# Optimization experiments

Hardware: AMD Instinct MI355X
Metric: run time of the kernel (lower is better)

The kernel has to match this reference:

```python
import math
import jax, jax.numpy as jnp
import numpy as np

DMODEL = 1024
NUM_HEADS = 16
HEAD_DIM = DMODEL // NUM_HEADS
MAX_LEN = 1024


def setup_inputs() -> dict:
    key = jax.random.key(0)
    ks = jax.random.split(key, 10)
    bs, S = 4, 1024
    s = 0.02
    return {
        "query": jax.random.normal(ks[0], (bs, S, DMODEL), jnp.float32),
        "key": jax.random.normal(ks[1], (bs, S, DMODEL), jnp.float32),
        "value": jax.random.normal(ks[2], (bs, S, DMODEL), jnp.float32),
        "Wq": jax.random.normal(ks[3], (DMODEL, DMODEL), jnp.float32) * s,
        "bq": jnp.zeros((DMODEL,), jnp.float32),
        "Wk": jax.random.normal(ks[4], (DMODEL, DMODEL), jnp.float32) * s,
        "bk": jnp.zeros((DMODEL,), jnp.float32),
        "Wv": jax.random.normal(ks[5], (DMODEL, DMODEL), jnp.float32) * s,
        "bv": jnp.zeros((DMODEL,), jnp.float32),
        # relative embedding table: (H, 2*max_len-1+2, head_dim)
        "Er": jax.random.normal(ks[6], (NUM_HEADS, 2 * MAX_LEN + 1, HEAD_DIM), jnp.float32),
    }


def _skew(QEr):
    # Music-Transformer skew trick. QEr: (bs, H, S, L) with L = 2S-1.
    bs, H, S, L = QEr.shape
    x = jnp.pad(QEr, ((0, 0), (0, 0), (0, 0), (0, 1)))          # (bs,H,S,L+1)
    x = x.reshape(bs, H, S * (L + 1))
    x = jnp.pad(x, ((0, 0), (0, 0), (0, L - S)))
    x = x.reshape(bs, H, S + 1, L)
    return x[:, :, :S, -S:]                                      # (bs,H,S,S)


def reference(query, key, value, Wq, bq, Wk, bk, Wv, bv, Er):
    bs, S, D = query.shape
    H, hd = NUM_HEADS, HEAD_DIM
    # torch nn.Linear: x @ W.T + b
    q = (query @ Wq.T + bq).reshape(bs, S, H, hd).transpose(0, 2, 1, 3)  # (bs,H,S,hd)
    k = (key @ Wk.T + bk).reshape(bs, S, H, hd).transpose(0, 2, 1, 3)    # (bs,H,S,hd)
    v = (value @ Wv.T + bv).reshape(bs, S, H, hd).transpose(0, 2, 1, 3)  # (bs,H,S,hd)
    # slice Er for src_len <= max_len: rows [max_len-S, max_len+S-1) -> (H, 2S-1, hd)
    Er_t = Er[:, max(0, MAX_LEN - S):min(2 * MAX_LEN - 1, MAX_LEN + S - 1), :]
    QEr = jnp.einsum('bhsd,hld->bhsl', q, Er_t)                  # (bs,H,S,2S-1)
    Srel = _skew(QEr)                                            # (bs,H,S,S)
    attn = (jnp.einsum('bhsd,bhtd->bhst', q, k) + Srel) / math.sqrt(hd)
    attn = jax.nn.softmax(attn, axis=-1)
    out = jnp.einsum('bhst,bhtd->bhsd', attn, v)                 # (bs,H,S,hd)
    out = out.transpose(0, 2, 1, 3).reshape(bs, S, D)
    return out, attn
```

## Files before the change

### kernel.cpp

```cpp
#include <hip/hip_runtime.h>
#include <hip/hip_fp16.h>

#define SQ   1024
#define DM   1024
#define NH   16
#define HD   64
#define BSZ  4
#define MROW 4096

typedef _Float16 f16;
typedef f16  f16x8 __attribute__((ext_vector_type(8)));
typedef float f32x4 __attribute__((ext_vector_type(4)));

#define MFMA16(a,b,c) __builtin_amdgcn_mfma_f32_16x16x32_f16(a,b,c,0,0,0)

#define XIN16OFF  0
#define W16OFF    12582912
#define ER16OFF   15728640
#define QKV16OFF  17826816

__global__ __launch_bounds__(256) void cvt_all(
    const float* __restrict__ q, const float* __restrict__ k, const float* __restrict__ v,
    const float* __restrict__ wq, const float* __restrict__ wk, const float* __restrict__ wv,
    const float* __restrict__ er, f16* __restrict__ ws)
{
    int z = blockIdx.z;
    const float* src; f16* dst; int n;
    if (z < 3)      { src = (z==0)?q:((z==1)?k:v);    dst = ws + (size_t)z*4194304;              n = 4194304; }
    else if (z < 6) { src = (z==3)?wq:((z==4)?wk:wv); dst = ws + W16OFF + (size_t)(z-3)*1048576; n = 1048576; }
    else            { src = er;                        dst = ws + ER16OFF;                        n = 2098176; }
    int idx = (blockIdx.x*256 + threadIdx.x) * 8;
    if (idx >= n) return;
    float4 a = *(const float4*)&src[idx];
    float4 b = *(const float4*)&src[idx+4];
    f16x8 o;
    o[0]=(f16)a.x; o[1]=(f16)a.y; o[2]=(f16)a.z; o[3]=(f16)a.w;
    o[4]=(f16)b.x; o[5]=(f16)b.y; o[6]=(f16)b.z; o[7]=(f16)b.w;
    *(f16x8*)&dst[idx] = o;
}

__global__ __launch_bounds__(256) void proj_gemm(
    f16* __restrict__ ws, const float* __restrict__ bq,
    const float* __restrict__ bk, const float* __restrict__ bv)
{
    int z = blockIdx.z;
    const f16* X = ws + XIN16OFF + (size_t)z*4194304;
    const f16* W = ws + W16OFF   + (size_t)z*1048576;
    const float* bias = (z==0)?bq:((z==1)?bk:bv);
    f16* dst = ws + QKV16OFF + (size_t)z*4194304;

    int n0 = blockIdx.x * 64, m0 = blockIdx.y * 64;
    int tid = threadIdx.x, lane = tid & 63, w = tid >> 6;
    int wm = (w >> 1) * 32, wn = (w & 1) * 32;

    __shared__ f16 As[64*40];
    __shared__ f16 Bs[64*40];

    f32x4 acc[2][2];
    #pragma unroll
    for (int a=0;a<2;++a) for (int b=0;b<2;++b) { acc[a][b][0]=0.f;acc[a][b][1]=0.f;acc[a][b][2]=0.f;acc[a][b][3]=0.f; }

    int row = tid >> 2, kc = (tid & 3) * 8;
    int fr = lane & 15, fk = (lane >> 4) << 3;

    for (int k0 = 0; k0 < 1024; k0 += 32) {
        __syncthreads();
        *(f16x8*)&As[row*40 + kc] = *(const f16x8*)&X[(size_t)(m0+row)*1024 + k0 + kc];
        *(f16x8*)&Bs[row*40 + kc] = *(const f16x8*)&W[(size_t)(n0+row)*1024 + k0 + kc];
        __syncthreads();
        f16x8 af[2], bf[2];
        af[0] = *(const f16x8*)&As[(wm +      fr)*40 + fk];
        af[1] = *(const f16x8*)&As[(wm + 16 + fr)*40 + fk];
        bf[0] = *(const f16x8*)&Bs[(wn +      fr)*40 + fk];
        bf[1] = *(const f16x8*)&Bs[(wn + 16 + fr)*40 + fk];
        #pragma unroll
        for (int a=0;a<2;++a)
            #pragma unroll
            for (int b=0;b<2;++b)
                acc[a][b] = MFMA16(af[a], bf[b], acc[a][b]);
    }

    int coln = lane & 15, rq = (lane >> 4) << 2;
    #pragma unroll
    for (int bb = 0; bb < 2; ++bb) {
        int j = n0 + wn + bb*16 + coln;
        int hh = j >> 6, dd = j & 63;
        float bsv = bias[j];
        #pragma unroll
        for (int a = 0; a < 2; ++a) {
            #pragma unroll
            for (int r = 0; r < 4; ++r) {
                int m = m0 + wm + a*16 + rq + r;
                int bidx = m >> 10, s = m & 1023;
                dst[((size_t)(bidx*16 + hh)*1024 + s)*64 + dd] = (f16)(acc[a][bb][r] + bsv);
            }
        }
    }
}

__global__ __launch_bounds__(256) void attn_kernel(
    const f16* __restrict__ ws, float* __restrict__ attn)
{
    const f16* qkv = ws + QKV16OFF;
    const f16* er  = ws + ER16OFF;
    int bh = blockIdx.y;
    int h  = bh & 15;
    int s0 = blockIdx.x << 4;
    int tid = threadIdx.x, lane = tid & 63, w = tid >> 6;

    const f16* qb = qkv + (size_t)bh * 65536;
    const f16* kb = qkv + 4194304 + (size_t)bh * 65536;
    const f16* E  = er + (size_t)h * 2049 * 64;

    int fr = lane & 15, fk = (lane >> 4) << 3;
    f16x8 qf0 = *(const f16x8*)&qb[(s0+fr)*64 + fk];
    f16x8 qf1 = *(const f16x8*)&qb[(s0+fr)*64 + fk + 32];

    int tbase = w << 8;
    f32x4 sc[16];
    int l0 = 1008 + tbase - s0;
    f16x8 e0a = *(const f16x8*)&E[(size_t)(l0+fr)*64 + fk];
    f16x8 e0b = *(const f16x8*)&E[(size_t)(l0+fr)*64 + fk + 32];

    #pragma unroll
    for (int i = 0; i < 16; ++i) {
        int t0 = tbase + (i << 4);
        f16x8 kf0 = *(const f16x8*)&kb[(t0+fr)*64 + fk];
        f16x8 kf1 = *(const f16x8*)&kb[(t0+fr)*64 + fk + 32];
        f32x4 c; c[0]=0.f;c[1]=0.f;c[2]=0.f;c[3]=0.f;
        c = MFMA16(qf0, kf0, c);
        c = MFMA16(qf1, kf1, c);

        int l1 = l0 + 16;
        f16x8 e1a = *(const f16x8*)&E[(size_t)(l1+fr)*64 + fk];
        f16x8 e1b = *(const f16x8*)&E[(size_t)(l1+fr)*64 + fk + 32];
        f32x4 r0; r0[0]=0.f;r0[1]=0.f;r0[2]=0.f;r0[3]=0.f;
        f32x4 r1; r1[0]=0.f;r1[1]=0.f;r1[2]=0.f;r1[3]=0.f;
        r0 = MFMA16(qf0, e0a, r0); r0 = MFMA16(qf1, e0b, r0);
        r1 = MFMA16(qf0, e1a, r1); r1 = MFMA16(qf1, e1b, r1);

        #pragma unroll
        for (int r = 0; r < 4; ++r) {
            int shat = ((lane >> 4) << 2) + r;
            int jj = (lane & 15) - shat + 15;
            int addr = ((lane & 48) | (jj & 15)) << 2;
            float g0 = __int_as_float(__builtin_amdgcn_ds_bpermute(addr, __float_as_int(r0[r])));
            float g1 = __int_as_float(__builtin_amdgcn_ds_bpermute(addr, __float_as_int(r1[r])));
            c[r] = (c[r] + ((jj < 16) ? g0 : g1)) * 0.125f;
        }
        sc[i] = c;
        e0a = e1a; e0b = e1b; l0 = l1;
    }

    __shared__ float red[16][4];
    float mx[4];
    #pragma unroll
    for (int r = 0; r < 4; ++r) {
        float m = sc[0][r];
        #pragma unroll
        for (int i = 1; i < 16; ++i) m = fmaxf(m, sc[i][r]);
        m = fmaxf(m, __shfl_xor(m, 1));
        m = fmaxf(m, __shfl_xor(m, 2));
        m = fmaxf(m, __shfl_xor(m, 4));
        m = fmaxf(m, __shfl_xor(m, 8));
        mx[r] = m;
    }
    if ((lane & 15) == 0) {
        #pragma unroll
        for (int r = 0; r < 4; ++r) red[((lane>>4)<<2)+r][w] = mx[r];
    }
    __syncthreads();
    #pragma unroll
    for (int r = 0; r < 4; ++r) {
        int rw = ((lane>>4)<<2)+r;
        mx[r] = fmaxf(fmaxf(red[rw][0], red[rw][1]), fmaxf(red[rw][2], red[rw][3]));
    }
    __syncthreads();
    float sm[4];
    #pragma unroll
    for (int r = 0; r < 4; ++r) {
        float s = 0.f;
        #pragma unroll
        for (int i = 0; i < 16; ++i) { float e = __expf(sc[i][r] - mx[r]); sc[i][r] = e; s += e; }
        s += __shfl_xor(s, 1); s += __shfl_xor(s, 2);
        s += __shfl_xor(s, 4); s += __shfl_xor(s, 8);
        sm[r] = s;
    }
    if ((lane & 15) == 0) {
        #pragma unroll
        for (int r = 0; r < 4; ++r) red[((lane>>4)<<2)+r][w] = sm[r];
    }
    __syncthreads();
    float inv[4];
    #pragma unroll
    for (int r = 0; r < 4; ++r) {
        int rw = ((lane>>4)<<2)+r;
        inv[r] = 1.f / (red[rw][0] + red[rw][1] + red[rw][2] + red[rw][3]);
    }

    float* outb = attn + ((size_t)bh * 1024 + s0) * 1024;
    #pragma unroll
    for (int i = 0; i < 16; ++i) {
        int t = tbase + (i << 4) + (lane & 15);
        #pragma unroll
        for (int r = 0; r < 4; ++r) {
            int rw = ((lane>>4)<<2)+r;
            outb[(size_t)rw * 1024 + t] = sc[i][r] * inv[r];
        }
    }
}

__global__ __launch_bounds__(256) void pv_kernel(
    const float* __restrict__ attn, const f16* __restrict__ ws, float* __restrict__ out)
{
    const f16* vbase = ws + QKV16OFF + 2*4194304;
    int bh = blockIdx.y, h = bh & 15, b = bh >> 4;
    int s0 = blockIdx.x << 6;
    int tid = threadIdx.x, lane = tid & 63, w = tid >> 6;
    const f16* v = vbase + (size_t)bh * 65536;
    const float* arow = attn + ((size_t)bh * 1024 + s0 + (w<<4)) * 1024;

    __shared__ f16 vt[64*40];
    f32x4 acc[4];
    #pragma unroll
    for (int nb=0;nb<4;++nb) { acc[nb][0]=0.f;acc[nb][1]=0.f;acc[nb][2]=0.f;acc[nb][3]=0.f; }

    int fr = lane & 15, fk = (lane >> 4) << 3;
    int tt = tid >> 3, dd = (tid & 7) << 3;

    for (int t0 = 0; t0 < 1024; t0 += 32) {
        __syncthreads();
        f16x8 vv = *(const f16x8*)&v[(size_t)(t0+tt)*64 + dd];
        #pragma unroll
        for (int j = 0; j < 8; ++j) vt[(dd+j)*40 + tt] = vv[j];
        __syncthreads();

        float4 a0 = *(const float4*)&arow[(size_t)fr*1024 + t0 + fk];
        float4 a1 = *(const float4*)&arow[(size_t)fr*1024 + t0 + fk + 4];
        f16x8 af;
        af[0]=(f16)(a0.x*512.f); af[1]=(f16)(a0.y*512.f); af[2]=(f16)(a0.z*512.f); af[3]=(f16)(a0.w*512.f);
        af[4]=(f16)(a1.x*512.f); af[5]=(f16)(a1.y*512.f); af[6]=(f16)(a1.z*512.f); af[7]=(f16)(a1.w*512.f);

        #pragma unroll
        for (int nb = 0; nb < 4; ++nb) {
            f16x8 bf = *(const f16x8*)&vt[((nb<<4)+fr)*40 + fk];
            acc[nb] = MFMA16(af, bf, acc[nb]);
        }
    }

    float* ob = out + ((size_t)b * 1024 + s0 + (w<<4)) * 1024 + h*64;
    int col = lane & 15;
    #pragma unroll
    for (int nb = 0; nb < 4; ++nb) {
        #pragma unroll
        for (int r = 0; r < 4; ++r) {
            int rw = ((lane>>4)<<2) + r;
            ob[(size_t)rw*1024 + (nb<<4) + col] = acc[nb][r] * (1.f/512.f);
        }
    }
}

extern "C" void kernel_launch(void* const* d_in, const int* in_sizes, int n_in,
                              void* d_out, int out_size, void* d_ws, size_t ws_size,
                              hipStream_t stream) {
    const float* query = (const float*)d_in[0];
    const float* key   = (const float*)d_in[1];
    const float* value = (const float*)d_in[2];
    const float* Wq    = (const float*)d_in[3];
    const float* bq    = (const float*)d_in[4];
    const float* Wk    = (const float*)d_in[5];
    const float* bk    = (const float*)d_in[6];
    const float* Wv    = (const float*)d_in[7];
    const float* bv    = (const float*)d_in[8];
    const float* Er    = (const float*)d_in[9];

    f16*   ws   = (f16*)d_ws;
    float* out  = (float*)d_out;
    float* attn = out + 4194304;

    cvt_all  <<<dim3(2048, 1, 7), 256, 0, stream>>>(query, key, value, Wq, Wk, Wv, Er, ws);
    proj_gemm<<<dim3(16, 64, 3),  256, 0, stream>>>(ws, bq, bk, bv);
    attn_kernel<<<dim3(64, 64),   256, 0, stream>>>(ws, attn);
    pv_kernel<<<dim3(16, 64),     256, 0, stream>>>(attn, ws, out);
}
```

Measured before the change: 595.6 us.

## Fuse PV into attention kernel, enlarge projection GEMM tiles, pre-transpose V

The separate PV kernel, which re-read the fp32 attention matrix from global memory, is removed. The attention kernel now keeps unnormalized fp16 probabilities in LDS, writes the normalized attn output from there, and multiplies by a pre-transposed V, reducing the partial outputs of the four waves through LDS. The projection GEMM moves to 128x128 tiles with a 4x4 MFMA block per wave and direct global-to-LDS loads. A small transpose kernel for V is added, and the LDS layout drops the padding, which can cause bank conflicts.

New measurement: 561.8 us. 1.06x faster.

```diff
diff --git a/kernel.cpp b/kernel.cpp
--- a/kernel.cpp
+++ b/kernel.cpp
@@ -6,18 +6,22 @@
 #define NH   16
 #define HD   64
 #define BSZ  4
-#define MROW 4096
 
 typedef _Float16 f16;
 typedef f16  f16x8 __attribute__((ext_vector_type(8)));
 typedef float f32x4 __attribute__((ext_vector_type(4)));
 
 #define MFMA16(a,b,c) __builtin_amdgcn_mfma_f32_16x16x32_f16(a,b,c,0,0,0)
+
+#define GLOAD_LDS(g, l) __builtin_amdgcn_global_load_lds( \
+    (const __attribute__((address_space(1))) void*)(g), \
+    (__attribute__((address_space(3))) void*)(l), 16, 0, 0)
 
 #define XIN16OFF  0
 #define W16OFF    12582912
 #define ER16OFF   15728640
 #define QKV16OFF  17826816
+#define VTOFF     30409728
 
 __global__ __launch_bounds__(256) void cvt_all(
     const float* __restrict__ q, const float* __restrict__ k, const float* __restrict__ v,
@@ -49,68 +53,98 @@
     const float* bias = (z==0)?bq:((z==1)?bk:bv);
     f16* dst = ws + QKV16OFF + (size_t)z*4194304;
 
-    int n0 = blockIdx.x * 64, m0 = blockIdx.y * 64;
+    int n0 = blockIdx.x * 128, m0 = blockIdx.y * 128;
     int tid = threadIdx.x, lane = tid & 63, w = tid >> 6;
-    int wm = (w >> 1) * 32, wn = (w & 1) * 32;
-
-    __shared__ f16 As[64*40];
-    __shared__ f16 Bs[64*40];
-
-    f32x4 acc[2][2];
-    #pragma unroll
-    for (int a=0;a<2;++a) for (int b=0;b<2;++b) { acc[a][b][0]=0.f;acc[a][b][1]=0.f;acc[a][b][2]=0.f;acc[a][b][3]=0.f; }
-
-    int row = tid >> 2, kc = (tid & 3) * 8;
+    int wm = (w >> 1) * 64, wn = (w & 1) * 64;
+
+    __shared__ f16 As[128*32];
+    __shared__ f16 Bs[128*32];
+
+    f32x4 acc[4][4];
+    #pragma unroll
+    for (int a=0;a<4;++a)
+        #pragma unroll
+        for (int b=0;b<4;++b) { acc[a][b][0]=0.f;acc[a][b][1]=0.f;acc[a][b][2]=0.f;acc[a][b][3]=0.f; }
+
+    int srow0 = tid >> 2, srow1 = srow0 + 64, skc = (tid & 3) * 8;
     int fr = lane & 15, fk = (lane >> 4) << 3;
 
     for (int k0 = 0; k0 < 1024; k0 += 32) {
         __syncthreads();
-        *(f16x8*)&As[row*40 + kc] = *(const f16x8*)&X[(size_t)(m0+row)*1024 + k0 + kc];
-        *(f16x8*)&Bs[row*40 + kc] = *(const f16x8*)&W[(size_t)(n0+row)*1024 + k0 + kc];
+        GLOAD_LDS(&X[(size_t)(m0+srow0)*1024 + k0 + skc], &As[srow0*32 + skc]);
+        GLOAD_LDS(&X[(size_t)(m0+srow1)*1024 + k0 + skc], &As[srow1*32 + skc]);
+        GLOAD_LDS(&W[(size_t)(n0+srow0)*1024 + k0 + skc], &Bs[srow0*32 + skc]);
+        GLOAD_LDS(&W[(size_t)(n0+srow1)*1024 + k0 + skc], &Bs[srow1*32 + skc]);
         __syncthreads();
-        f16x8 af[2], bf[2];
-        af[0] = *(const f16x8*)&As[(wm +      fr)*40 + fk];
-        af[1] = *(const f16x8*)&As[(wm + 16 + fr)*40 + fk];
-        bf[0] = *(const f16x8*)&Bs[(wn +      fr)*40 + fk];
-        bf[1] = *(const f16x8*)&Bs[(wn + 16 + fr)*40 + fk];
-        #pragma unroll
-        for (int a=0;a<2;++a)
+        f16x8 af[4], bf[4];
+        #pragma unroll
+        for (int a=0;a<4;++a) af[a] = *(const f16x8*)&As[(wm + a*16 + fr)*32 + fk];
+        #pragma unroll
+        for (int b=0;b<4;++b) bf[b] = *(const f16x8*)&Bs[(wn + b*16 + fr)*32 + fk];
+        #pragma unroll
+        for (int a=0;a<4;++a)
             #pragma unroll
-            for (int b=0;b<2;++b)
+            for (int b=0;b<4;++b)
                 acc[a][b] = MFMA16(af[a], bf[b], acc[a][b]);
     }
 
     int coln = lane & 15, rq = (lane >> 4) << 2;
     #pragma unroll
-    for (int bb = 0; bb < 2; ++bb) {
-        int j = n0 + wn + bb*16 + coln;
+    for (int tb = 0; tb < 4; ++tb) {
+        int j = n0 + wn + tb*16 + coln;
         int hh = j >> 6, dd = j & 63;
         float bsv = bias[j];
         #pragma unroll
-        for (int a = 0; a < 2; ++a) {
+        for (int ta = 0; ta < 4; ++ta) {
             #pragma unroll
             for (int r = 0; r < 4; ++r) {
-                int m = m0 + wm + a*16 + rq + r;
+                int m = m0 + wm + ta*16 + rq + r;
                 int bidx = m >> 10, s = m & 1023;
-                dst[((size_t)(bidx*16 + hh)*1024 + s)*64 + dd] = (f16)(acc[a][bb][r] + bsv);
+                dst[((size_t)(bidx*16 + hh)*1024 + s)*64 + dd] = (f16)(acc[ta][tb][r] + bsv);
             }
         }
     }
 }
 
-__global__ __launch_bounds__(256) void attn_kernel(
-    const f16* __restrict__ ws, float* __restrict__ attn)
+__global__ __launch_bounds__(256) void transpose_v(f16* __restrict__ ws)
+{
+    const f16* v = ws + QKV16OFF + 2*4194304 + (size_t)blockIdx.y*65536;
+    f16* o       = ws + VTOFF               + (size_t)blockIdx.y*65536;
+    int s0 = blockIdx.x << 6;
+    __shared__ f16 t[64][72];
+    int tid = threadIdx.x;
+    int r = tid >> 2, c = (tid & 3) << 4;
+    f16x8 a = *(const f16x8*)&v[(size_t)(s0+r)*64 + c];
+    f16x8 b = *(const f16x8*)&v[(size_t)(s0+r)*64 + c + 8];
+    #pragma unroll
+    for (int j = 0; j < 8; ++j) { t[r][c+j] = a[j]; t[r][c+8+j] = b[j]; }
+    __syncthreads();
+    int dr = tid >> 2, sc0 = (tid & 3) << 4;
+    f16x8 o1, o2;
+    #pragma unroll
+    for (int j = 0; j < 8; ++j) { o1[j] = t[sc0+j][dr]; o2[j] = t[sc0+8+j][dr]; }
+    *(f16x8*)&o[(size_t)dr*1024 + s0 + sc0]     = o1;
+    *(f16x8*)&o[(size_t)dr*1024 + s0 + sc0 + 8] = o2;
+}
+
+__global__ __launch_bounds__(256) void attn_pv(
+    const f16* __restrict__ ws, float* __restrict__ attn, float* __restrict__ out)
 {
     const f16* qkv = ws + QKV16OFF;
     const f16* er  = ws + ER16OFF;
-    int bh = blockIdx.y;
-    int h  = bh & 15;
+    int bh = blockIdx.y, h = bh & 15, b = bh >> 4;
     int s0 = blockIdx.x << 4;
     int tid = threadIdx.x, lane = tid & 63, w = tid >> 6;
 
-    const f16* qb = qkv + (size_t)bh * 65536;
-    const f16* kb = qkv + 4194304 + (size_t)bh * 65536;
-    const f16* E  = er + (size_t)h * 2049 * 64;
+    const f16* qb  = qkv + (size_t)bh * 65536;
+    const f16* kb  = qkv + 4194304 + (size_t)bh * 65536;
+    const f16* vtb = ws + VTOFF + (size_t)bh * 65536;
+    const f16* E   = er + (size_t)h * 2049 * 64;
+
+    __shared__ __align__(16) f16 lds_pool[4*16*264];
+    __shared__ float red[16][4];
+    __shared__ float invs[16];
+    f16* P16 = lds_pool + w * (16*264);
 
     int fr = lane & 15, fk = (lane >> 4) << 3;
     f16x8 qf0 = *(const f16x8*)&qb[(s0+fr)*64 + fk];
@@ -152,7 +186,6 @@
         e0a = e1a; e0b = e1b; l0 = l1;
     }
 
-    __shared__ float red[16][4];
     float mx[4];
     #pragma unroll
     for (int r = 0; r < 4; ++r) {
@@ -179,9 +212,14 @@
     float sm[4];
     #pragma unroll
     for (int r = 0; r < 4; ++r) {
+        int rw = ((lane>>4)<<2)+r;
         float s = 0.f;
         #pragma unroll
-        for (int i = 0; i < 16; ++i) { float e = __expf(sc[i][r] - mx[r]); sc[i][r] = e; s += e; }
+        for (int i = 0; i < 16; ++i) {
+            float e = __expf(sc[i][r] - mx[r]);
+            s += e;
+            P16[rw*264 + (i<<4) + (lane & 15)] = (f16)e;
+        }
         s += __shfl_xor(s, 1); s += __shfl_xor(s, 2);
         s += __shfl_xor(s, 4); s += __shfl_xor(s, 8);
         sm[r] = s;
@@ -191,72 +229,67 @@
         for (int r = 0; r < 4; ++r) red[((lane>>4)<<2)+r][w] = sm[r];
     }
     __syncthreads();
-    float inv[4];
-    #pragma unroll
-    for (int r = 0; r < 4; ++r) {
-        int rw = ((lane>>4)<<2)+r;
-        inv[r] = 1.f / (red[rw][0] + red[rw][1] + red[rw][2] + red[rw][3]);
-    }
-
-    float* outb = attn + ((size_t)bh * 1024 + s0) * 1024;
-    #pragma unroll
-    for (int i = 0; i < 16; ++i) {
-        int t = tbase + (i << 4) + (lane & 15);
+    if (w == 0 && (lane & 15) == 0) {
         #pragma unroll
         for (int r = 0; r < 4; ++r) {
             int rw = ((lane>>4)<<2)+r;
-            outb[(size_t)rw * 1024 + t] = sc[i][r] * inv[r];
-        }
-    }
-}
-
-__global__ __launch_bounds__(256) void pv_kernel(
-    const float* __restrict__ attn, const f16* __restrict__ ws, float* __restrict__ out)
-{
-    const f16* vbase = ws + QKV16OFF + 2*4194304;
-    int bh = blockIdx.y, h = bh & 15, b = bh >> 4;
-    int s0 = blockIdx.x << 6;
-    int tid = threadIdx.x, lane = tid & 63, w = tid >> 6;
-    const f16* v = vbase + (size_t)bh * 65536;
-    const float* arow = attn + ((size_t)bh * 1024 + s0 + (w<<4)) * 1024;
-
-    __shared__ f16 vt[64*40];
-    f32x4 acc[4];
-    #pragma unroll
-    for (int nb=0;nb<4;++nb) { acc[nb][0]=0.f;acc[nb][1]=0.f;acc[nb][2]=0.f;acc[nb][3]=0.f; }
-
-    int fr = lane & 15, fk = (lane >> 4) << 3;
-    int tt = tid >> 3, dd = (tid & 7) << 3;
-
-    for (int t0 = 0; t0 < 1024; t0 += 32) {
-        __syncthreads();
-        f16x8 vv = *(const f16x8*)&v[(size_t)(t0+tt)*64 + dd];
-        #pragma unroll
-        for (int j = 0; j < 8; ++j) vt[(dd+j)*40 + tt] = vv[j];
-        __syncthreads();
-
-        float4 a0 = *(const float4*)&arow[(size_t)fr*1024 + t0 + fk];
-        float4 a1 = *(const float4*)&arow[(size_t)fr*1024 + t0 + fk + 4];
-        f16x8 af;
-        af[0]=(f16)(a0.x*512.f); af[1]=(f16)(a0.y*512.f); af[2]=(f16)(a0.z*512.f); af[3]=(f16)(a0.w*512.f);
-        af[4]=(f16)(a1.x*512.f); af[5]=(f16)(a1.y*512.f); af[6]=(f16)(a1.z*512.f); af[7]=(f16)(a1.w*512.f);
-
+            invs[rw] = 1.f / (red[rw][0] + red[rw][1] + red[rw][2] + red[rw][3]);
+        }
+    }
+    __syncthreads();
+
+    {
+        float* outb = attn + ((size_t)bh * 1024 + s0) * 1024;
+        int arow = tid >> 4;
+        int ac0  = (tid & 15) << 2;
+        float iv = invs[arow];
+        #pragma unroll
+        for (int it = 0; it < 16; ++it) {
+            int col = ac0 + it*64;
+            const f16* p = &lds_pool[(col >> 8)*(16*264) + arow*264 + (col & 255)];
+            float4 o4;
+            o4.x = (float)p[0] * iv; o4.y = (float)p[1] * iv;
+            o4.z = (float)p[2] * iv; o4.w = (float)p[3] * iv;
+            *(float4*)&outb[(size_t)arow*1024 + col] = o4;
+        }
+    }
+
+    f32x4 oacc[4];
+    #pragma unroll
+    for (int nb=0;nb<4;++nb) { oacc[nb][0]=0.f;oacc[nb][1]=0.f;oacc[nb][2]=0.f;oacc[nb][3]=0.f; }
+    #pragma unroll
+    for (int kc = 0; kc < 8; ++kc) {
+        f16x8 af = *(const f16x8*)&P16[fr*264 + (kc<<5) + fk];
         #pragma unroll
         for (int nb = 0; nb < 4; ++nb) {
-            f16x8 bf = *(const f16x8*)&vt[((nb<<4)+fr)*40 + fk];
-            acc[nb] = MFMA16(af, bf, acc[nb]);
-        }
-    }
-
-    float* ob = out + ((size_t)b * 1024 + s0 + (w<<4)) * 1024 + h*64;
-    int col = lane & 15;
-    #pragma unroll
-    for (int nb = 0; nb < 4; ++nb) {
-        #pragma unroll
-        for (int r = 0; r < 4; ++r) {
-            int rw = ((lane>>4)<<2) + r;
-            ob[(size_t)rw*1024 + (nb<<4) + col] = acc[nb][r] * (1.f/512.f);
-        }
+            f16x8 bf = *(const f16x8*)&vtb[(size_t)((nb<<4)+fr)*1024 + tbase + (kc<<5) + fk];
+            oacc[nb] = MFMA16(af, bf, oacc[nb]);
+        }
+    }
+
+    __syncthreads();
+    float* Ored = (float*)lds_pool;
+    {
+        float iv2[4];
+        #pragma unroll
+        for (int r = 0; r < 4; ++r) iv2[r] = invs[((lane>>4)<<2)+r];
+        #pragma unroll
+        for (int nb = 0; nb < 4; ++nb)
+            #pragma unroll
+            for (int r = 0; r < 4; ++r) {
+                int rw = ((lane>>4)<<2)+r;
+                Ored[w*1024 + rw*64 + (nb<<4) + (lane & 15)] = oacc[nb][r] * iv2[r];
+            }
+    }
+    __syncthreads();
+    {
+        int frow = tid >> 4, fc = (tid & 15) << 2;
+        float4 s4;
+        s4.x = Ored[frow*64+fc+0] + Ored[1024+frow*64+fc+0] + Ored[2048+frow*64+fc+0] + Ored[3072+frow*64+fc+0];
+        s4.y = Ored[frow*64+fc+1] + Ored[1024+frow*64+fc+1] + Ored[2048+frow*64+fc+1] + Ored[3072+frow*64+fc+1];
+        s4.z = Ored[frow*64+fc+2] + Ored[1024+frow*64+fc+2] + Ored[2048+frow*64+fc+2] + Ored[3072+frow*64+fc+2];
+        s4.w = Ored[frow*64+fc+3] + Ored[1024+frow*64+fc+3] + Ored[2048+frow*64+fc+3] + Ored[3072+frow*64+fc+3];
+        *(float4*)&out[((size_t)b*1024 + s0 + frow)*1024 + h*64 + fc] = s4;
     }
 }
 
@@ -272,14 +305,14 @@
     const float* bk    = (const float*)d_in[6];
     const float* Wv    = (const float*)d_in[7];
     const float* bv    = (const float*)d_in[8];
-    const float* Er    = (const float*)d_in[9];
 
     f16*   ws   = (f16*)d_ws;
     float* out  = (float*)d_out;
     float* attn = out + 4194304;
 
-    cvt_all  <<<dim3(2048, 1, 7), 256, 0, stream>>>(query, key, value, Wq, Wk, Wv, Er, ws);
-    proj_gemm<<<dim3(16, 64, 3),  256, 0, stream>>>(ws, bq, bk, bv);
-    attn_kernel<<<dim3(64, 64),   256, 0, stream>>>(ws, attn);
-    pv_kernel<<<dim3(16, 64),     256, 0, stream>>>(attn, ws, out);
-}
+    cvt_all    <<<dim3(2048, 1, 7), 256, 0, stream>>>(query, key, value, Wq, Wk, Wv,
+                                                      (const float*)d_in[9], ws);
+    proj_gemm  <<<dim3(8, 32, 3),   256, 0, stream>>>(ws, bq, bk, bv);
+    transpose_v<<<dim3(16, 64),     256, 0, stream>>>(ws);
+    attn_pv    <<<dim3(64, 64),     256, 0, stream>>>(ws, attn, out);
+}
```
